# Performance work log

Hardware: AMD Instinct MI355X
Metric: run time of the kernel (lower is better)

## Reference

```python
import jax, jax.numpy as jnp
import numpy as np

B, S, D, H = 2, 2048, 1024, 16
HD = D // H          # 64
HALF = HD // 2       # 32
EPS = 1e-6           # RMSNorm eps (module default eps=1e-6)


def setup_inputs() -> dict:
    key = jax.random.key(0)
    ks = jax.random.split(key, 6)
    x = jax.random.normal(ks[0], (B, S, D), jnp.float32)
    scale = 1.0 / np.sqrt(D)
    Wq = jax.random.normal(ks[1], (D, D), jnp.float32) * scale
    Wk = jax.random.normal(ks[2], (D, D), jnp.float32) * scale
    Wv = jax.random.normal(ks[3], (D, D), jnp.float32) * scale
    Wo = jax.random.normal(ks[4], (D, D), jnp.float32) * scale
    bq = jnp.zeros((D,), jnp.float32)
    bk = jnp.zeros((D,), jnp.float32)
    bv = jnp.zeros((D,), jnp.float32)
    bo = jnp.zeros((D,), jnp.float32)
    gq = jnp.ones((D,), jnp.float32)   # norm_q weight
    gk = jnp.ones((D,), jnp.float32)   # norm_k weight
    # Standard RoPE angles: pos * 10000^(-2i/head_dim); freqs = exp(i*ang)
    pos = jnp.arange(S, dtype=jnp.float32)
    inv_freq = 1.0 / (10000.0 ** (jnp.arange(0, HD, 2, dtype=jnp.float32) / HD))
    ang = pos[:, None] * inv_freq[None, :]          # (S, HALF)
    return dict(x=x, Wq=Wq, bq=bq, Wk=Wk, bk=bk, Wv=Wv, bv=bv, Wo=Wo, bo=bo,
                gq=gq, gk=gk, freqs_cos=jnp.cos(ang), freqs_sin=jnp.sin(ang))


def _rmsnorm(x, g):
    # x * rsqrt(mean(x^2) + eps) * g, computed in fp32 as in the torch module
    return x * jax.lax.rsqrt(jnp.mean(x * x, axis=-1, keepdims=True) + EPS) * g


def _rope(x, cos, sin):
    # x: (B,S,D) packed heads; rotate consecutive (even,odd) pairs per head.
    xr = x.reshape(B, S, H, HALF, 2)
    x0, x1 = xr[..., 0], xr[..., 1]
    c = cos[None, :, None, :]  # (1,S,1,HALF)
    s = sin[None, :, None, :]
    o0 = x0 * c - x1 * s
    o1 = x0 * s + x1 * c
    return jnp.stack([o0, o1], axis=-1).reshape(B, S, D)


def reference(x, Wq, bq, Wk, bk, Wv, bv, Wo, bo, gq, gk, freqs_cos, freqs_sin):
    q = _rmsnorm(x @ Wq.T + bq, gq)
    k = _rmsnorm(x @ Wk.T + bk, gk)
    v = x @ Wv.T + bv
    q = _rope(q, freqs_cos, freqs_sin)
    k = _rope(k, freqs_cos, freqs_sin)
    # SDPA (non-causal, as F.scaled_dot_product_attention default call)
    qh = q.reshape(B, S, H, HD)
    kh = k.reshape(B, S, H, HD)
    vh = v.reshape(B, S, H, HD)
    scores = jnp.einsum('bqhd,bkhd->bhqk', qh, kh) / np.sqrt(HD)
    attn = jax.nn.softmax(scores, axis=-1)
    out = jnp.einsum('bhqk,bkhd->bqhd', attn, vh).reshape(B, S, D)
    return out @ Wo.T + bo
```

## Files before the change

### kernel.cpp

```cpp
#include <hip/hip_runtime.h>

typedef unsigned short u16;
typedef unsigned int u32;
typedef u16 u16x4 __attribute__((ext_vector_type(4)));
typedef u16 u16x8 __attribute__((ext_vector_type(8)));
typedef u32 u32x4 __attribute__((ext_vector_type(4)));
typedef float f32x4 __attribute__((ext_vector_type(4)));
typedef float f32x16 __attribute__((ext_vector_type(16)));
typedef __bf16 bf16x2 __attribute__((ext_vector_type(2)));
typedef __bf16 bf16x8 __attribute__((ext_vector_type(8)));

#define GLOAD16(gp, lp)                                             \
  __builtin_amdgcn_global_load_lds(                                 \
      (const __attribute__((address_space(1))) void*)(gp),          \
      (__attribute__((address_space(3))) void*)(lp), 16, 0, 0)

__device__ __forceinline__ u16 f2bf(float f) {
  unsigned int u = __builtin_bit_cast(unsigned int, f);
  u += 0x7FFFu + ((u >> 16) & 1u);
  return (u16)(u >> 16);
}
__device__ __forceinline__ float bf2f(u16 h) {
  return __builtin_bit_cast(float, (u32)h << 16);
}

__global__ __launch_bounds__(256) void f2b_kernel(const float* __restrict__ in,
                                                  u16* __restrict__ out, int n4) {
  int i = blockIdx.x * 256 + threadIdx.x;
  if (i < n4) {
    f32x4 v = *(const f32x4*)(in + (size_t)i * 4);
    u16x4 o;
    o[0] = f2bf(v[0]); o[1] = f2bf(v[1]); o[2] = f2bf(v[2]); o[3] = f2bf(v[3]);
    *(u16x4*)(out + (size_t)i * 4) = o;
  }
}

__global__ __launch_bounds__(256) void f2bw_kernel(const float* __restrict__ s0,
    const float* __restrict__ s1, const float* __restrict__ s2,
    const float* __restrict__ s3, u16* __restrict__ dst) {
  const int y = blockIdx.y;
  const float* s = (y == 0) ? s0 : ((y == 1) ? s1 : ((y == 2) ? s2 : s3));
  int i = blockIdx.x * 256 + threadIdx.x;
  f32x4 v = *(const f32x4*)(s + (size_t)i * 4);
  u16x4 o;
  o[0] = f2bf(v[0]); o[1] = f2bf(v[1]); o[2] = f2bf(v[2]); o[3] = f2bf(v[3]);
  *(u16x4*)(dst + (size_t)y * 1048576 + (size_t)i * 4) = o;
}

__device__ __forceinline__ void gemm_core(const u16* __restrict__ A,
                                          const u16* __restrict__ W,
                                          int bm0, int bn0,
                                          u16* ldsA, u16* ldsB,
                                          f32x4 acc[4][4]) {
  const int tid = threadIdx.x;
  const int l = tid & 63;
  const int lr = l & 15, lk = l >> 4;
  const int w = tid >> 6;
  const int wr = w >> 1, wc = w & 1;
  const int srow = tid >> 2, sko = (tid & 3) << 3;
  auto stage = [&](int kt, int buf) {
#pragma unroll
    for (int it = 0; it < 2; ++it) {
      int row = it * 64 + srow;
      GLOAD16(A + (size_t)(bm0 + row) * 1024 + kt * 32 + sko,
              ldsA + buf * 4096 + (it * 256 + tid) * 8);
      GLOAD16(W + (size_t)(bn0 + row) * 1024 + kt * 32 + sko,
              ldsB + buf * 4096 + (it * 256 + tid) * 8);
    }
  };
  stage(0, 0);
  stage(1, 1);
  int cur = 0, nx2 = 2;
  for (int kt = 0; kt < 32; ++kt) {
    if (kt < 31) asm volatile("s_waitcnt vmcnt(4)" ::: "memory");
    else         asm volatile("s_waitcnt vmcnt(0)" ::: "memory");
    __builtin_amdgcn_s_barrier();
    __builtin_amdgcn_sched_barrier(0);
    if (kt + 2 < 32) stage(kt + 2, nx2);
    const u16* lA = ldsA + cur * 4096;
    const u16* lB = ldsB + cur * 4096;
    bf16x8 af[4], bfr[4];
#pragma unroll
    for (int m = 0; m < 4; ++m)
      af[m] = *(const bf16x8*)(lA + (wr * 64 + m * 16 + lr) * 32 + lk * 8);
#pragma unroll
    for (int n = 0; n < 4; ++n)
      bfr[n] = *(const bf16x8*)(lB + (wc * 64 + n * 16 + lr) * 32 + lk * 8);
#pragma unroll
    for (int m = 0; m < 4; ++m)
#pragma unroll
      for (int n = 0; n < 4; ++n)
        acc[m][n] = __builtin_amdgcn_mfma_f32_16x16x32_bf16(af[m], bfr[n], acc[m][n], 0, 0, 0);
    cur = (cur == 2) ? 0 : cur + 1;
    nx2 = (nx2 == 2) ? 0 : nx2 + 1;
  }
}

__global__ __launch_bounds__(256) void qkv_gemm(const u16* __restrict__ xb,
    const u16* __restrict__ wq, const u16* __restrict__ wk, const u16* __restrict__ wv,
    const float* __restrict__ bq, const float* __restrict__ bk, const float* __restrict__ bv,
    u16* __restrict__ Qb, u16* __restrict__ Kb, u16* __restrict__ Vf) {
  __shared__ u16 ldsA[3 * 4096];
  __shared__ u16 ldsB[3 * 4096];
  const int z = blockIdx.z;
  const u16* W = (z == 0) ? wq : ((z == 1) ? wk : wv);
  const float* bias = (z == 0) ? bq : ((z == 1) ? bk : bv);
  const int bm0 = blockIdx.x * 128, bn0 = blockIdx.y * 128;
  const f32x4 zf = {0.f, 0.f, 0.f, 0.f};
  f32x4 acc[4][4];
#pragma unroll
  for (int m = 0; m < 4; ++m)
#pragma unroll
    for (int n = 0; n < 4; ++n) acc[m][n] = zf;
  gemm_core(xb, W, bm0, bn0, ldsA, ldsB, acc);
  const int tid = threadIdx.x, l = tid & 63, lr = l & 15, lk = l >> 4;
  const int w = tid >> 6, wr = w >> 1, wc = w & 1;
  float bcol[4];
#pragma unroll
  for (int n = 0; n < 4; ++n) bcol[n] = bias[bn0 + wc * 64 + n * 16 + lr];
  if (z < 2) {
    u16* outp = z ? Kb : Qb;
#pragma unroll
    for (int m = 0; m < 4; ++m)
#pragma unroll
      for (int n = 0; n < 4; ++n)
#pragma unroll
        for (int r = 0; r < 4; ++r) {
          int row = bm0 + wr * 64 + m * 16 + lk * 4 + r;
          int col = bn0 + wc * 64 + n * 16 + lr;
          outp[(size_t)row * 1024 + col] = f2bf(acc[m][n][r] + bcol[n]);
        }
  } else {
#pragma unroll
    for (int m = 0; m < 4; ++m)
#pragma unroll
      for (int n = 0; n < 4; ++n) {
        int row = bm0 + wr * 64 + m * 16 + lk * 4;
        int col = bn0 + wc * 64 + n * 16 + lr;
        int b = row >> 11, sf = row & 2047, hh = col >> 6, hd = col & 63;
        int t = sf >> 6, kin = sf & 63;
        int ks = kin >> 4, hiv = (kin >> 3) & 1, j0 = kin & 7;
        int vhalf = hd >> 5, lq = hd & 31;
        u16x4 o;
#pragma unroll
        for (int r = 0; r < 4; ++r) o[r] = f2bf(acc[m][n][r] + bcol[n]);
        size_t addr = (size_t)(b * 16 + hh) * 131072 +
                      (size_t)(((t * 4 + ks) * 2 + vhalf)) * 512 +
                      ((hiv << 5) + lq) * 8 + j0;
        *(u16x4*)(Vf + addr) = o;
      }
  }
}

__global__ __launch_bounds__(256) void proj_gemm(const u16* __restrict__ ctx,
    const u16* __restrict__ wo, const float* __restrict__ bo, float* __restrict__ out) {
  __shared__ u16 ldsA[3 * 4096];
  __shared__ u16 ldsB[3 * 4096];
  const int bm0 = blockIdx.x * 128, bn0 = blockIdx.y * 128;
  const f32x4 zf = {0.f, 0.f, 0.f, 0.f};
  f32x4 acc[4][4];
#pragma unroll
  for (int m = 0; m < 4; ++m)
#pragma unroll
    for (int n = 0; n < 4; ++n) acc[m][n] = zf;
  gemm_core(ctx, wo, bm0, bn0, ldsA, ldsB, acc);
  const int tid = threadIdx.x, l = tid & 63, lr = l & 15, lk = l >> 4;
  const int w = tid >> 6, wr = w >> 1, wc = w & 1;
  float bcol[4];
#pragma unroll
  for (int n = 0; n < 4; ++n) bcol[n] = bo[bn0 + wc * 64 + n * 16 + lr];
#pragma unroll
  for (int m = 0; m < 4; ++m)
#pragma unroll
    for (int n = 0; n < 4; ++n)
#pragma unroll
      for (int r = 0; r < 4; ++r) {
        int row = bm0 + wr * 64 + m * 16 + lk * 4 + r;
        int col = bn0 + wc * 64 + n * 16 + lr;
        out[(size_t)row * 1024 + col] = acc[m][n][r] + bcol[n];
      }
}

__global__ __launch_bounds__(256) void rmsrope(const u16* __restrict__ Qb,
    const u16* __restrict__ Kb, const float* __restrict__ gq, const float* __restrict__ gk,
    const float* __restrict__ fc, const float* __restrict__ fs,
    u16* __restrict__ Qf, u16* __restrict__ Kf) {
  const int row = blockIdx.x;
  const int which = blockIdx.y;
  const u16* src = (which ? Kb : Qb) + (size_t)row * 1024;
  const float* g = which ? gk : gq;
  const int t = threadIdx.x;
  u16x4 raw = *(const u16x4*)(src + t * 4);
  float v0 = bf2f(raw[0]), v1 = bf2f(raw[1]), v2 = bf2f(raw[2]), v3 = bf2f(raw[3]);
  float ss = v0 * v0 + v1 * v1 + v2 * v2 + v3 * v3;
#pragma unroll
  for (int mm = 1; mm < 64; mm <<= 1) ss += __shfl_xor(ss, mm);
  __shared__ float red[4];
  if ((t & 63) == 0) red[t >> 6] = ss;
  __syncthreads();
  float rstd = rsqrtf((red[0] + red[1] + red[2] + red[3]) * (1.0f / 1024.0f) + 1e-6f);
  if (!which) rstd *= 0.18033688011112042f;
  int d = t * 4, hh = d >> 6, dh = d & 63, p = dh >> 1;
  int s = row & 2047, b = row >> 11;
  float c0 = fc[(s << 5) + p], s0 = fs[(s << 5) + p];
  float c1 = fc[(s << 5) + p + 1], s1 = fs[(s << 5) + p + 1];
  float x0 = v0 * rstd * g[d];
  float x1 = v1 * rstd * g[d + 1];
  float x2 = v2 * rstd * g[d + 2];
  float x3 = v3 * rstd * g[d + 3];
  u16x4 o;
  o[0] = f2bf(x0 * c0 - x1 * s0);
  o[1] = f2bf(x0 * s0 + x1 * c0);
  o[2] = f2bf(x2 * c1 - x3 * s1);
  o[3] = f2bf(x2 * s1 + x3 * c1);
  const size_t base = (size_t)(b * 16 + hh) * 131072;
  const int hs = dh >> 4, hi = (dh >> 3) & 1, j0 = dh & 7;
  size_t addr;
  if (!which) {
    addr = base + (size_t)((s >> 5) * 4 + hs) * 512 + ((hi << 5) + (s & 31)) * 8 + j0;
  } else {
    addr = base + (size_t)(((s >> 6) * 4 + hs) * 2 + ((s >> 5) & 1)) * 512 +
           ((hi << 5) + (s & 31)) * 8 + j0;
  }
  *(u16x4*)((which ? Kf : Qf) + addr) = o;
}

__global__ __launch_bounds__(256, 2) void attn_kernel(const u16* __restrict__ Qf,
    const u16* __restrict__ Kf, const u16* __restrict__ Vf, u16* __restrict__ ctx) {
  const int tid = threadIdx.x;
  const int w = tid >> 6, l = tid & 63;
  const int lq = l & 31, hi = l >> 5;
  const bool hiB = (hi != 0);
  const int id = blockIdx.x;
  const int qt = (id >> 3) & 15;
  const int hb = (id & 7) | ((id >> 7) << 3);
  const int h = hb & 15, b = hb >> 4;
  const int bh = b * 16 + h;
  const u16* Qp = Qf + (size_t)bh * 131072;
  const u16* Kp = Kf + (size_t)bh * 131072;
  const u16* Vp = Vf + (size_t)bh * 131072;
  bf16x8 qf[4];
#pragma unroll
  for (int hs = 0; hs < 4; ++hs)
    qf[hs] = *(const bf16x8*)(Qp + (size_t)((qt * 4 + w) * 4 + hs) * 512 + l * 8);

  auto ldK = [&](int t, bf16x8* kr) {
#pragma unroll
    for (int i = 0; i < 8; ++i)
      kr[i] = *(const bf16x8*)(Kp + ((size_t)t * 8 + i) * 512 + l * 8);
  };
  auto ldV = [&](int t, bf16x8* vr) {
#pragma unroll
    for (int i = 0; i < 8; ++i)
      vr[i] = *(const bf16x8*)(Vp + ((size_t)t * 8 + i) * 512 + l * 8);
  };

  const f32x16 z16 = {0,0,0,0, 0,0,0,0, 0,0,0,0, 0,0,0,0};
  f32x16 O0 = z16, O1 = z16;
  float lsum = 0.f;

  auto qk_step = [&](const bf16x8* kr, f32x16& s0, f32x16& s1) {
    s0 = z16; s1 = z16;
    __builtin_amdgcn_s_setprio(1);
#pragma unroll
    for (int hs = 0; hs < 4; ++hs) {
      s0 = __builtin_amdgcn_mfma_f32_32x32x16_bf16(kr[hs * 2 + 0], qf[hs], s0, 0, 0, 0);
      s1 = __builtin_amdgcn_mfma_f32_32x32x16_bf16(kr[hs * 2 + 1], qf[hs], s1, 0, 0, 0);
    }
    __builtin_amdgcn_s_setprio(0);
  };

  auto sm_pv = [&](const bf16x8* vr, f32x16& sc0, f32x16& sc1) {
    float rs = 0.f;
    u32 pk0[8], pk1[8];
#pragma unroll
    for (int m = 0; m < 8; ++m) {
      float a0 = exp2f(sc0[2 * m]), a1 = exp2f(sc0[2 * m + 1]);
      float c0 = exp2f(sc1[2 * m]), c1 = exp2f(sc1[2 * m + 1]);
      rs += (a0 + a1) + (c0 + c1);
      bf16x2 pA; pA[0] = (__bf16)a0; pA[1] = (__bf16)a1;
      bf16x2 pC; pC[0] = (__bf16)c0; pC[1] = (__bf16)c1;
      pk0[m] = __builtin_bit_cast(u32, pA);
      pk1[m] = __builtin_bit_cast(u32, pC);
    }
    rs += __shfl_xor(rs, 32);
    lsum += rs;
    auto xchg = [&](u32 X, u32 Y, u32& wlo, u32& whi) {
      u32 s1v = hiB ? X : Y;
      u32 r = (u32)__shfl_xor((int)s1v, 32);
      wlo = hiB ? r : X;
      whi = hiB ? Y : r;
    };
    bf16x8 pb[4];
    {
      u32 w0, w1, w2, w3;
      xchg(pk0[0], pk0[2], w0, w2);
      xchg(pk0[1], pk0[3], w1, w3);
      u32x4 pw = {w0, w1, w2, w3};
      pb[0] = __builtin_bit_cast(bf16x8, pw);
      xchg(pk0[4], pk0[6], w0, w2);
      xchg(pk0[5], pk0[7], w1, w3);
      u32x4 pw1 = {w0, w1, w2, w3};
      pb[1] = __builtin_bit_cast(bf16x8, pw1);
      xchg(pk1[0], pk1[2], w0, w2);
      xchg(pk1[1], pk1[3], w1, w3);
      u32x4 pw2 = {w0, w1, w2, w3};
      pb[2] = __builtin_bit_cast(bf16x8, pw2);
      xchg(pk1[4], pk1[6], w0, w2);
      xchg(pk1[5], pk1[7], w1, w3);
      u32x4 pw3 = {w0, w1, w2, w3};
      pb[3] = __builtin_bit_cast(bf16x8, pw3);
    }
    __builtin_amdgcn_s_setprio(1);
#pragma unroll
    for (int ks = 0; ks < 4; ++ks) {
      O0 = __builtin_amdgcn_mfma_f32_32x32x16_bf16(vr[ks * 2 + 0], pb[ks], O0, 0, 0, 0);
      O1 = __builtin_amdgcn_mfma_f32_32x32x16_bf16(vr[ks * 2 + 1], pb[ks], O1, 0, 0, 0);
    }
    __builtin_amdgcn_s_setprio(0);
  };

  bf16x8 kA[8], kB[8], vA[8], vB[8];
  f32x16 scX0, scX1;
  ldK(0, kA);
  ldV(0, vA);
#pragma unroll 1
  for (int dt = 0; dt < 16; ++dt) {
    int t = dt * 2;
    {
      ldK(t + 1, kB);
      ldV(t + 1, vB);
      qk_step(kA, scX0, scX1);
      sm_pv(vA, scX0, scX1);
    }
    {
      if (dt < 15) { ldK(t + 2, kA); ldV(t + 2, vA); }
      qk_step(kB, scX0, scX1);
      sm_pv(vB, scX0, scX1);
    }
  }
  float inv = 1.0f / lsum;
  const int q0 = qt * 128 + w * 32;
  const size_t rowoff = ((size_t)(b * 2048 + q0 + lq)) * 1024 + h * 64;
#pragma unroll
  for (int g = 0; g < 4; ++g) {
    u16x4 oa, ob;
#pragma unroll
    for (int rr = 0; rr < 4; ++rr) {
      oa[rr] = f2bf(O0[4 * g + rr] * inv);
      ob[rr] = f2bf(O1[4 * g + rr] * inv);
    }
    *(u16x4*)(ctx + rowoff + 8 * g + 4 * hi) = oa;
    *(u16x4*)(ctx + rowoff + 32 + 8 * g + 4 * hi) = ob;
  }
}

extern "C" void kernel_launch(void* const* d_in, const int* in_sizes, int n_in,
                              void* d_out, int out_size, void* d_ws, size_t ws_size,
                              hipStream_t stream) {
  (void)in_sizes; (void)n_in; (void)out_size; (void)ws_size;
  const float* x  = (const float*)d_in[0];
  const float* Wq = (const float*)d_in[1];
  const float* bq = (const float*)d_in[2];
  const float* Wk = (const float*)d_in[3];
  const float* bk = (const float*)d_in[4];
  const float* Wv = (const float*)d_in[5];
  const float* bv = (const float*)d_in[6];
  const float* Wo = (const float*)d_in[7];
  const float* bo = (const float*)d_in[8];
  const float* gq = (const float*)d_in[9];
  const float* gk = (const float*)d_in[10];
  const float* fc = (const float*)d_in[11];
  const float* fs = (const float*)d_in[12];
  float* out = (float*)d_out;
  char* ws = (char*)d_ws;
  u16*  xb  = (u16*)(ws + 0);
  u16*  wqb = (u16*)(ws + 8388608);
  u16*  wkb = (u16*)(ws + 10485760);
  u16*  wvb = (u16*)(ws + 12582912);
  u16*  wob = (u16*)(ws + 14680064);
  u16*  Qfb = (u16*)(ws + 16777216);
  u16*  Kfb = (u16*)(ws + 25165824);
  u16*  Qfr = (u16*)(ws + 33554432);
  u16*  Kfr = (u16*)(ws + 41943040);
  u16*  Vfr = (u16*)(ws + 50331648);
  u16*  ctx = (u16*)(ws + 58720256);

  f2b_kernel<<<4096, 256, 0, stream>>>(x, xb, 1048576);
  f2bw_kernel<<<dim3(1024, 4), 256, 0, stream>>>(Wq, Wk, Wv, Wo, wqb);
  qkv_gemm<<<dim3(32, 8, 3), 256, 0, stream>>>(xb, wqb, wkb, wvb, bq, bk, bv, Qfb, Kfb, Vfr);
  rmsrope<<<dim3(4096, 2), 256, 0, stream>>>(Qfb, Kfb, gq, gk, fc, fs, Qfr, Kfr);
  attn_kernel<<<512, 256, 0, stream>>>(Qfr, Kfr, Vfr, ctx);
  proj_gemm<<<dim3(32, 8), 256, 0, stream>>>(ctx, wob, bo, out);
}
```

Baseline: 145.2 us.

## Split attention KV range across two wave groups and combine in LDS

```diff
diff --git a/kernel.cpp b/kernel.cpp
--- a/kernel.cpp
+++ b/kernel.cpp
@@ -225,10 +225,12 @@
   *(u16x4*)((which ? Kf : Qf) + addr) = o;
 }
 
-__global__ __launch_bounds__(256, 2) void attn_kernel(const u16* __restrict__ Qf,
+__global__ __launch_bounds__(512, 4) void attn_kernel(const u16* __restrict__ Qf,
     const u16* __restrict__ Kf, const u16* __restrict__ Vf, u16* __restrict__ ctx) {
+  __shared__ float cmb[4][64][34];
   const int tid = threadIdx.x;
   const int w = tid >> 6, l = tid & 63;
+  const int wh = w & 3, ws = w >> 2;
   const int lq = l & 31, hi = l >> 5;
   const bool hiB = (hi != 0);
   const int id = blockIdx.x;
@@ -242,7 +244,7 @@
   bf16x8 qf[4];
 #pragma unroll
   for (int hs = 0; hs < 4; ++hs)
-    qf[hs] = *(const bf16x8*)(Qp + (size_t)((qt * 4 + w) * 4 + hs) * 512 + l * 8);
+    qf[hs] = *(const bf16x8*)(Qp + (size_t)((qt * 4 + wh) * 4 + hs) * 512 + l * 8);
 
   auto ldK = [&](int t, bf16x8* kr) {
 #pragma unroll
@@ -322,11 +324,12 @@
 
   bf16x8 kA[8], kB[8], vA[8], vB[8];
   f32x16 scX0, scX1;
-  ldK(0, kA);
-  ldV(0, vA);
+  const int t0 = ws * 16;
+  ldK(t0, kA);
+  ldV(t0, vA);
 #pragma unroll 1
-  for (int dt = 0; dt < 16; ++dt) {
-    int t = dt * 2;
+  for (int dt = 0; dt < 8; ++dt) {
+    int t = t0 + dt * 2;
     {
       ldK(t + 1, kB);
       ldV(t + 1, vB);
@@ -334,24 +337,41 @@
       sm_pv(vA, scX0, scX1);
     }
     {
-      if (dt < 15) { ldK(t + 2, kA); ldV(t + 2, vA); }
+      if (dt < 7) { ldK(t + 2, kA); ldV(t + 2, vA); }
       qk_step(kB, scX0, scX1);
       sm_pv(vB, scX0, scX1);
     }
   }
-  float inv = 1.0f / lsum;
-  const int q0 = qt * 128 + w * 32;
-  const size_t rowoff = ((size_t)(b * 2048 + q0 + lq)) * 1024 + h * 64;
-#pragma unroll
-  for (int g = 0; g < 4; ++g) {
-    u16x4 oa, ob;
-#pragma unroll
-    for (int rr = 0; rr < 4; ++rr) {
-      oa[rr] = f2bf(O0[4 * g + rr] * inv);
-      ob[rr] = f2bf(O1[4 * g + rr] * inv);
-    }
-    *(u16x4*)(ctx + rowoff + 8 * g + 4 * hi) = oa;
-    *(u16x4*)(ctx + rowoff + 32 + 8 * g + 4 * hi) = ob;
+  if (ws == 1) {
+#pragma unroll
+    for (int i = 0; i < 16; ++i) {
+      cmb[wh][l][i] = O0[i];
+      cmb[wh][l][16 + i] = O1[i];
+    }
+    cmb[wh][l][32] = lsum;
+  }
+  __syncthreads();
+  if (ws == 0) {
+#pragma unroll
+    for (int i = 0; i < 16; ++i) {
+      O0[i] += cmb[wh][l][i];
+      O1[i] += cmb[wh][l][16 + i];
+    }
+    lsum += cmb[wh][l][32];
+    float inv = 1.0f / lsum;
+    const int q0 = qt * 128 + wh * 32;
+    const size_t rowoff = ((size_t)(b * 2048 + q0 + lq)) * 1024 + h * 64;
+#pragma unroll
+    for (int g = 0; g < 4; ++g) {
+      u16x4 oa, ob;
+#pragma unroll
+      for (int rr = 0; rr < 4; ++rr) {
+        oa[rr] = f2bf(O0[4 * g + rr] * inv);
+        ob[rr] = f2bf(O1[4 * g + rr] * inv);
+      }
+      *(u16x4*)(ctx + rowoff + 8 * g + 4 * hi) = oa;
+      *(u16x4*)(ctx + rowoff + 32 + 8 * g + 4 * hi) = ob;
+    }
   }
 }
 
@@ -390,6 +410,6 @@
   f2bw_kernel<<<dim3(1024, 4), 256, 0, stream>>>(Wq, Wk, Wv, Wo, wqb);
   qkv_gemm<<<dim3(32, 8, 3), 256, 0, stream>>>(xb, wqb, wkb, wvb, bq, bk, bv, Qfb, Kfb, Vfr);
   rmsrope<<<dim3(4096, 2), 256, 0, stream>>>(Qfb, Kfb, gq, gk, fc, fs, Qfr, Kfr);
-  attn_kernel<<<512, 256, 0, stream>>>(Qfr, Kfr, Vfr, ctx);
+  attn_kernel<<<512, 512, 0, stream>>>(Qfr, Kfr, Vfr, ctx);
   proj_gemm<<<dim3(32, 8), 256, 0, stream>>>(ctx, wob, bo, out);
 }
```

New measurement: 329.2 us. 2.27x slower.

## Software-pipeline QK of next tile with softmax-PV of current in attention

Applied to the files above, without the earlier changes.

```diff
diff --git a/kernel.cpp b/kernel.cpp
--- a/kernel.cpp
+++ b/kernel.cpp
@@ -225,7 +225,7 @@
   *(u16x4*)((which ? Kf : Qf) + addr) = o;
 }
 
-__global__ __launch_bounds__(256, 2) void attn_kernel(const u16* __restrict__ Qf,
+__global__ __launch_bounds__(256) void attn_kernel(const u16* __restrict__ Qf,
     const u16* __restrict__ Kf, const u16* __restrict__ Vf, u16* __restrict__ ctx) {
   const int tid = threadIdx.x;
   const int w = tid >> 6, l = tid & 63;
@@ -275,8 +275,10 @@
     u32 pk0[8], pk1[8];
 #pragma unroll
     for (int m = 0; m < 8; ++m) {
-      float a0 = exp2f(sc0[2 * m]), a1 = exp2f(sc0[2 * m + 1]);
-      float c0 = exp2f(sc1[2 * m]), c1 = exp2f(sc1[2 * m + 1]);
+      float a0 = __builtin_amdgcn_exp2f(sc0[2 * m]);
+      float a1 = __builtin_amdgcn_exp2f(sc0[2 * m + 1]);
+      float c0 = __builtin_amdgcn_exp2f(sc1[2 * m]);
+      float c1 = __builtin_amdgcn_exp2f(sc1[2 * m + 1]);
       rs += (a0 + a1) + (c0 + c1);
       bf16x2 pA; pA[0] = (__bf16)a0; pA[1] = (__bf16)a1;
       bf16x2 pC; pC[0] = (__bf16)c0; pC[1] = (__bf16)c1;
@@ -320,23 +322,28 @@
     __builtin_amdgcn_s_setprio(0);
   };
 
-  bf16x8 kA[8], kB[8], vA[8], vB[8];
-  f32x16 scX0, scX1;
-  ldK(0, kA);
-  ldV(0, vA);
+  bf16x8 kE[8], kO[8], vE[8], vO[8];
+  f32x16 scA0, scA1, scB0, scB1;
+  ldK(0, kE);
+  ldV(0, vE);
+  ldK(1, kO);
+  qk_step(kE, scA0, scA1);
 #pragma unroll 1
   for (int dt = 0; dt < 16; ++dt) {
-    int t = dt * 2;
+    const int t = dt * 2;
     {
-      ldK(t + 1, kB);
-      ldV(t + 1, vB);
-      qk_step(kA, scX0, scX1);
-      sm_pv(vA, scX0, scX1);
+      if (t + 2 < 32) ldK(t + 2, kE);
+      ldV(t + 1, vO);
+      qk_step(kO, scB0, scB1);
+      sm_pv(vE, scA0, scA1);
     }
     {
-      if (dt < 15) { ldK(t + 2, kA); ldV(t + 2, vA); }
-      qk_step(kB, scX0, scX1);
-      sm_pv(vB, scX0, scX1);
+      if (t + 3 < 32) ldK(t + 3, kO);
+      if (t + 2 < 32) {
+        ldV(t + 2, vE);
+        qk_step(kE, scA0, scA1);
+      }
+      sm_pv(vO, scB0, scB1);
     }
   }
   float inv = 1.0f / lsum;
```

Result: no change. 143.5 us (-1.2%).
